# Optimization experiments

Measured on AMD Instinct MI355X. Metric: run time of the kernel, lower is better.

The kernel has to match this reference:

```python
import jax, jax.numpy as jnp
import numpy as np

HEADS = 8
AGENT = 49
POOL = 7   # sqrt(AGENT)
WIN = 32


def _adaptive_avg_pool(x, out):
    # x: (b, h, w, c) -> (b, out, out, c), replicating torch AdaptiveAvgPool2d bins
    h = x.shape[1]
    starts = [(i * h) // out for i in range(out)]
    ends = [-((-(i + 1) * h) // out) for i in range(out)]
    rows = jnp.stack([x[:, s:e].mean(axis=1) for s, e in zip(starts, ends)], axis=1)      # (b,out,w,c)
    return jnp.stack([rows[:, :, s:e].mean(axis=2) for s, e in zip(starts, ends)], axis=2)  # (b,out,out,c)


def setup_inputs() -> dict:
    key = jax.random.key(0)
    ks = jax.random.split(key, 13)
    b, n, c = 32, WIN * WIN, 256
    std = 0.02
    return {
        "x": jax.random.normal(ks[0], (b, n + 1, c), jnp.float32),
        "qkv_w": jax.random.normal(ks[1], (3 * c, c), jnp.float32) * std,
        "proj_w": jax.random.normal(ks[2], (c, c), jnp.float32) * std,
        "proj_b": jnp.zeros((c,), jnp.float32),
        "dwc_w": jax.random.normal(ks[3], (c, 1, 3, 3), jnp.float32) * std,  # torch (C_out, 1, kh, kw)
        "dwc_b": jnp.zeros((c,), jnp.float32),
        "an_bias": jax.random.normal(ks[4], (HEADS, AGENT, 7, 7), jnp.float32) * std,
        "ah_bias": jax.random.normal(ks[5], (1, HEADS, AGENT, WIN, 1), jnp.float32) * std,
        "aw_bias": jax.random.normal(ks[6], (1, HEADS, AGENT, 1, WIN), jnp.float32) * std,
        "na_bias": jax.random.normal(ks[7], (HEADS, AGENT, 7, 7), jnp.float32) * std,
        "ha_bias": jax.random.normal(ks[8], (1, HEADS, WIN, 1, AGENT), jnp.float32) * std,
        "wa_bias": jax.random.normal(ks[9], (1, HEADS, 1, WIN, AGENT), jnp.float32) * std,
    }


def reference(x, qkv_w, proj_w, proj_b, dwc_w, dwc_b,
              an_bias, ah_bias, aw_bias, na_bias, ha_bias, wa_bias):
    cls_tok, xs = x[:, :1], x[:, 1:]
    b, n, c = xs.shape
    h = w = WIN
    hd = c // HEADS
    scale = hd ** -0.5

    qkv = xs @ qkv_w.T                                   # (b, n, 3c)
    q, k, v = jnp.split(qkv, 3, axis=-1)                 # each (b, n, c)

    # agent tokens: adaptive avg pool of q over the spatial grid
    agents = _adaptive_avg_pool(q.reshape(b, h, w, c), POOL).reshape(b, AGENT, c)

    qh = q.reshape(b, n, HEADS, hd).transpose(0, 2, 1, 3)        # (b,H,n,d)
    kh = k.reshape(b, n, HEADS, hd).transpose(0, 2, 1, 3)
    vh = v.reshape(b, n, HEADS, hd).transpose(0, 2, 1, 3)
    ah = agents.reshape(b, AGENT, HEADS, hd).transpose(0, 2, 1, 3)  # (b,H,A,d)

    # stage 1: agent <-> k/v, bias interpolated 7x7 -> WINxWIN (half-pixel bilinear == torch align_corners=False)
    pb1 = jax.image.resize(an_bias, (HEADS, AGENT, WIN, WIN), method='bilinear').reshape(1, HEADS, AGENT, n)
    pb2 = (ah_bias + aw_bias).reshape(1, HEADS, AGENT, n)
    agent_attn = jax.nn.softmax((ah * scale) @ kh.transpose(0, 1, 3, 2) + pb1 + pb2, axis=-1)  # (b,H,A,n)
    agent_v = agent_attn @ vh                                    # (b,H,A,d)

    # stage 2: q <-> agents
    ab1 = jax.image.resize(na_bias, (HEADS, AGENT, WIN, WIN), method='bilinear').reshape(1, HEADS, AGENT, n).transpose(0, 1, 3, 2)
    ab2 = (ha_bias + wa_bias).reshape(1, HEADS, n, AGENT)
    q_attn = jax.nn.softmax((qh * scale) @ ah.transpose(0, 1, 3, 2) + ab1 + ab2, axis=-1)      # (b,H,n,A)
    out = (q_attn @ agent_v).transpose(0, 2, 1, 3).reshape(b, n, c)

    # depthwise conv residual on v (NHWC)
    v_img = vh.transpose(0, 2, 1, 3).reshape(b, h, w, c)
    kern = dwc_w.transpose(2, 3, 1, 0)                            # (3,3,1,c) HWIO
    dwc = jax.lax.conv_general_dilated(v_img, kern, (1, 1), 'SAME',
                                       feature_group_count=c,
                                       dimension_numbers=('NHWC', 'HWIO', 'NHWC')) + dwc_b
    out = out + dwc.reshape(b, n, c)

    out = jnp.concatenate([cls_tok, out], axis=1)
    return out @ proj_w.T + proj_b
```

## Files before the change

kernel.cpp:

```cpp
#include <hip/hip_runtime.h>
#include <hip/hip_bf16.h>

#define BATCH 32
#define NTOK 1024
#define CH 256
#define HEADS 8
#define HD 32
#define AGENTS 49
#define WIN 32
#define QKV_N 768
#define SCALE 0.17677669529663687f

typedef unsigned short u16;
typedef __attribute__((ext_vector_type(8))) unsigned short u16x8;
typedef __attribute__((ext_vector_type(8))) short short8;
typedef __attribute__((ext_vector_type(4))) float f32x4;

__device__ __forceinline__ void gload_lds16(const void* g, const void* l) {
    __builtin_amdgcn_global_load_lds(
        (const __attribute__((address_space(1))) unsigned int*)g,
        (__attribute__((address_space(3))) unsigned int*)l, 16, 0, 0);
}

__device__ __forceinline__ u16 f2bf1(float f) {
    unsigned u = __builtin_bit_cast(unsigned, f);
    u += 0x7fffu + ((u >> 16) & 1u);
    return (u16)(u >> 16);
}
__device__ __forceinline__ float bf2f(u16 v) {
    unsigned u = ((unsigned)v) << 16;
    return __builtin_bit_cast(float, u);
}

__global__ void f2bf_kernel(const float* __restrict__ in, u16* __restrict__ out, int n8) {
    int i = blockIdx.x * 256 + threadIdx.x;
    if (i >= n8) return;
    float4 v0 = ((const float4*)in)[i * 2];
    float4 v1 = ((const float4*)in)[i * 2 + 1];
    u16x8 o;
    o[0] = f2bf1(v0.x); o[1] = f2bf1(v0.y); o[2] = f2bf1(v0.z); o[3] = f2bf1(v0.w);
    o[4] = f2bf1(v1.x); o[5] = f2bf1(v1.y); o[6] = f2bf1(v1.z); o[7] = f2bf1(v1.w);
    ((u16x8*)out)[i] = o;
}

__global__ __launch_bounds__(256) void gemm_bf16(const u16* __restrict__ A,
                                                 const u16* __restrict__ B,
                                                 float* __restrict__ C,
                                                 u16* __restrict__ C16,
                                                 int M, int N, int K,
                                                 const float* __restrict__ bias,
                                                 int amode) {
    __shared__ u16 As[128 * 32];
    __shared__ u16 Bs[128 * 32];
    const int tid = threadIdx.x;
    const int lane = tid & 63;
    const int wid = tid >> 6;
    const int row0 = blockIdx.x * 128, col0 = blockIdx.y * 128;
    const int wr = wid >> 1, wc = wid & 1;
    const int fr = lane & 15, fq = lane >> 4;

    f32x4 acc[4][4];
#pragma unroll
    for (int m = 0; m < 4; ++m)
#pragma unroll
        for (int n = 0; n < 4; ++n) acc[m][n] = (f32x4)(0.f);

    for (int k0 = 0; k0 < K; k0 += 32) {
#pragma unroll
        for (int r = 0; r < 2; ++r) {
            int trow = (tid >> 2) + r * 64;
            int tcol = (tid & 3) * 8;
            size_t aoff;
            int grow = row0 + trow;
            if (amode == 1) {
                int bb = grow >> 10, nn = grow & 1023;
                aoff = ((size_t)(bb * 1025 + nn + 1)) * 256 + (size_t)(k0 + tcol);
            } else {
                if (grow >= M) grow = M - 1;
                aoff = (size_t)grow * K + (size_t)(k0 + tcol);
            }
            gload_lds16(A + aoff, (const char*)As + wid * 1024 + r * 4096);
            int brow = col0 + trow;
            gload_lds16(B + (size_t)brow * K + (size_t)(k0 + tcol),
                        (const char*)Bs + wid * 1024 + r * 4096);
        }
        __syncthreads();

        short8 af[4], bf[4];
#pragma unroll
        for (int m = 0; m < 4; ++m)
            af[m] = *(const short8*)&As[(wr * 64 + m * 16 + fr) * 32 + fq * 8];
#pragma unroll
        for (int n = 0; n < 4; ++n)
            bf[n] = *(const short8*)&Bs[(wc * 64 + n * 16 + fr) * 32 + fq * 8];
#pragma unroll
        for (int m = 0; m < 4; ++m)
#pragma unroll
            for (int n = 0; n < 4; ++n)
                acc[m][n] = __builtin_amdgcn_mfma_f32_16x16x32_bf16(af[m], bf[n], acc[m][n], 0, 0, 0);
        __syncthreads();
    }

#pragma unroll
    for (int m = 0; m < 4; ++m) {
#pragma unroll
        for (int j = 0; j < 4; ++j) {
            int row = row0 + wr * 64 + m * 16 + fq * 4 + j;
            if (row < M) {
#pragma unroll
                for (int n = 0; n < 4; ++n) {
                    int col = col0 + wc * 64 + n * 16 + fr;
                    float v = acc[m][n][j];
                    if (bias) v += bias[col];
                    if (C16) C16[(size_t)row * N + col] = f2bf1(v);
                    else     C[(size_t)row * N + col] = v;
                }
            }
        }
    }
}

__global__ __launch_bounds__(256) void pool_kernel(const u16* __restrict__ qkvb,
                                                   float* __restrict__ agents) {
    int b = blockIdx.x / 7, py = blockIdx.x % 7;
    int ch = threadIdx.x;
    int ys = py * 32 / 7, ye = ((py + 1) * 32 + 6) / 7;
    float acc[7];
#pragma unroll
    for (int i = 0; i < 7; ++i) acc[i] = 0.f;
    for (int y = ys; y < ye; ++y) {
        const u16* rowp = qkvb + ((size_t)(b * NTOK + y * 32)) * QKV_N + ch;
#pragma unroll
        for (int PX = 0; PX < 7; ++PX) {
            const int xs = PX * 32 / 7, xe = ((PX + 1) * 32 + 6) / 7;
            float s = 0.f;
            for (int x = xs; x < xe; ++x) s += bf2f(rowp[(size_t)x * QKV_N]);
            acc[PX] += s;
        }
    }
    int rcnt = ye - ys;
#pragma unroll
    for (int PX = 0; PX < 7; ++PX) {
        const int xs = PX * 32 / 7, xe = ((PX + 1) * 32 + 6) / 7;
        agents[((size_t)(b * AGENTS + py * 7 + PX)) * CH + ch] =
            acc[PX] / (float)(rcnt * (xe - xs));
    }
}

__device__ inline float bilin7(const float* __restrict__ m, float sy, float sx) {
    float fy0 = floorf(sy), fx0 = floorf(sx);
    int y0 = (int)fy0, x0 = (int)fx0;
    float fy = sy - fy0, fx = sx - fx0;
    int y0c = min(max(y0, 0), 6), y1c = min(max(y0 + 1, 0), 6);
    int x0c = min(max(x0, 0), 6), x1c = min(max(x0 + 1, 0), 6);
    float v00 = m[y0c * 7 + x0c], v01 = m[y0c * 7 + x1c];
    float v10 = m[y1c * 7 + x0c], v11 = m[y1c * 7 + x1c];
    return (1.f - fy) * ((1.f - fx) * v00 + fx * v01) + fy * ((1.f - fx) * v10 + fx * v11);
}

__global__ void pb_kernel(const float* __restrict__ an, const float* __restrict__ ahb,
                          const float* __restrict__ awb, float* __restrict__ pba) {
    int h = blockIdx.x / AGENTS, a = blockIdx.x % AGENTS;
    const float* m = an + (h * AGENTS + a) * 49;
    for (int n = threadIdx.x; n < NTOK; n += 256) {
        int y = n >> 5, x = n & 31;
        float v = bilin7(m, (y + 0.5f) * (7.f / 32.f) - 0.5f, (x + 0.5f) * (7.f / 32.f) - 0.5f);
        v += ahb[(h * AGENTS + a) * 32 + y] + awb[(h * AGENTS + a) * 32 + x];
        pba[((size_t)(h * AGENTS + a)) * NTOK + n] = v;
    }
}

__global__ void ab_kernel(const float* __restrict__ na, const float* __restrict__ hab,
                          const float* __restrict__ wab, float* __restrict__ ab) {
    int idx = blockIdx.x * 256 + threadIdx.x;
    if (idx >= HEADS * NTOK * AGENTS) return;
    int h = idx / (NTOK * AGENTS);
    int r = idx % (NTOK * AGENTS);
    int n = r / AGENTS, a = r % AGENTS;
    int y = n >> 5, x = n & 31;
    const float* m = na + (h * AGENTS + a) * 49;
    float v = bilin7(m, (y + 0.5f) * (7.f / 32.f) - 0.5f, (x + 0.5f) * (7.f / 32.f) - 0.5f);
    v += hab[(h * 32 + y) * AGENTS + a] + wab[(h * 32 + x) * AGENTS + a];
    ab[idx] = v;
}

__global__ __launch_bounds__(512) void agent_attn3(const u16* __restrict__ qkvb,
                                                   const float* __restrict__ agents,
                                                   const float* __restrict__ pba,
                                                   float* __restrict__ agent_v) {
    int b = blockIdx.x >> 3, h = blockIdx.x & 7;
    int tid = threadIdx.x, lane = tid & 63, w = tid >> 6;
    const int fr = lane & 15, fq = lane >> 4;

#define VTP 1038
    __shared__ u16 ah_lds[64 * 32];
    __shared__ u16 Vt[32 * VTP];
    __shared__ float PO[8][2304];
    __shared__ float lsum_lds[8][64];

    u16*   Pw = (u16*)&PO[w][0];
    float* Ow = &PO[w][0];

    for (int li = tid; li < 64 * 32; li += 512) {
        int a = li >> 5, d = li & 31;
        float v = (a < AGENTS) ? agents[((size_t)(b * AGENTS + a)) * CH + h * HD + d] * SCALE : 0.f;
        ah_lds[li] = f2bf1(v);
    }
    for (int li = tid; li < NTOK * 4; li += 512) {
        int tok = li >> 2, d8 = (li & 3) * 8;
        u16x8 v = *(const u16x8*)&qkvb[((size_t)(b * NTOK + tok)) * QKV_N + 2 * CH + h * HD + d8];
#pragma unroll
        for (int j = 0; j < 8; ++j) Vt[(d8 + j) * VTP + tok] = v[j];
    }
    __syncthreads();

    short8 ahf[4];
#pragma unroll
    for (int mt = 0; mt < 4; ++mt)
        ahf[mt] = *(const short8*)&ah_lds[(mt * 16 + fr) * 32 + fq * 8];

    float lsum[4][4];
#pragma unroll
    for (int mt = 0; mt < 4; ++mt)
#pragma unroll
        for (int j = 0; j < 4; ++j) lsum[mt][j] = 0.f;
    f32x4 accO[4][2];
#pragma unroll
    for (int mt = 0; mt < 4; ++mt)
#pragma unroll
        for (int ntd = 0; ntd < 2; ++ntd) accO[mt][ntd] = (f32x4)(0.f);

    const float* pbh = pba + (size_t)h * AGENTS * NTOK;

#pragma unroll
    for (int c2 = 0; c2 < 2; ++c2) {
        int tb = w * 128 + c2 * 64;
        short8 kf[4];
#pragma unroll
        for (int nt = 0; nt < 4; ++nt)
            kf[nt] = *(const short8*)&qkvb[((size_t)(b * NTOK + tb + nt * 16 + fr)) * QKV_N + CH + h * HD + fq * 8];

        f32x4 accS[4];
#pragma unroll
        for (int mt = 0; mt < 4; ++mt) {
#pragma unroll
            for (int nt = 0; nt < 4; ++nt)
                accS[nt] = __builtin_amdgcn_mfma_f32_16x16x32_bf16(ahf[mt], kf[nt], (f32x4)(0.f), 0, 0, 0);
#pragma unroll
            for (int j = 0; j < 4; ++j) {
                int a = mt * 16 + fq * 4 + j;
                const float* pbrow = pbh + (size_t)min(a, AGENTS - 1) * NTOK + tb;
#pragma unroll
                for (int nt = 0; nt < 4; ++nt) {
                    float e = __expf(accS[nt][j] + pbrow[nt * 16 + fr]);
                    lsum[mt][j] += e;
                    Pw[a * 72 + nt * 16 + fr] = f2bf1(e);
                }
            }
        }

        asm volatile("s_waitcnt lgkmcnt(0)" ::: "memory");
        __builtin_amdgcn_sched_barrier(0);

        short8 pf[4][2], vf[2][2];
#pragma unroll
        for (int mt = 0; mt < 4; ++mt)
#pragma unroll
            for (int kc = 0; kc < 2; ++kc)
                pf[mt][kc] = *(const short8*)&Pw[(mt * 16 + fr) * 72 + kc * 32 + fq * 8];
#pragma unroll
        for (int ntd = 0; ntd < 2; ++ntd)
#pragma unroll
            for (int kc = 0; kc < 2; ++kc)
                vf[ntd][kc] = *(const short8*)&Vt[(ntd * 16 + fr) * VTP + tb + kc * 32 + fq * 8];

        asm volatile("s_waitcnt lgkmcnt(0)" ::: "memory");
        __builtin_amdgcn_sched_barrier(0);

#pragma unroll
        for (int mt = 0; mt < 4; ++mt)
#pragma unroll
            for (int kc = 0; kc < 2; ++kc)
#pragma unroll
                for (int ntd = 0; ntd < 2; ++ntd)
                    accO[mt][ntd] = __builtin_amdgcn_mfma_f32_16x16x32_bf16(pf[mt][kc], vf[ntd][kc], accO[mt][ntd], 0, 0, 0);
    }

#pragma unroll
    for (int mt = 0; mt < 4; ++mt)
#pragma unroll
        for (int j = 0; j < 4; ++j) {
            float s = lsum[mt][j];
            s += __shfl_xor(s, 1);
            s += __shfl_xor(s, 2);
            s += __shfl_xor(s, 4);
            s += __shfl_xor(s, 8);
            lsum[mt][j] = s;
        }
    if (fr == 0) {
#pragma unroll
        for (int mt = 0; mt < 4; ++mt)
#pragma unroll
            for (int j = 0; j < 4; ++j)
                lsum_lds[w][mt * 16 + fq * 4 + j] = lsum[mt][j];
    }

#pragma unroll
    for (int mt = 0; mt < 4; ++mt)
#pragma unroll
        for (int ntd = 0; ntd < 2; ++ntd)
#pragma unroll
            for (int j = 0; j < 4; ++j)
                Ow[(mt * 16 + fq * 4 + j) * 32 + ntd * 16 + fr] = accO[mt][ntd][j];

    asm volatile("s_waitcnt lgkmcnt(0)" ::: "memory");
    __syncthreads();

    for (int li = tid; li < AGENTS * HD; li += 512) {
        int a = li >> 5, d = li & 31;
        float L = 0.f, o = 0.f;
#pragma unroll
        for (int ww = 0; ww < 8; ++ww) {
            o += PO[ww][a * 32 + d];
            L += lsum_lds[ww][a];
        }
        agent_v[(((size_t)(b * HEADS + h)) * AGENTS + a) * HD + d] = o / L;
    }
#undef VTP
}

__global__ __launch_bounds__(256) void q_attn_dwc(const u16* __restrict__ qkvb,
                                                  const float* __restrict__ agents,
                                                  const float* __restrict__ agent_v,
                                                  const float* __restrict__ ab,
                                                  const float* __restrict__ dwc_w,
                                                  const float* __restrict__ dwc_b,
                                                  u16* __restrict__ outbf) {
    int blk = blockIdx.x;
    int b = blk / 32, rem = blk % 32;
    int h = rem / 4, ck = rem % 4;
    int tid = threadIdx.x;
    int w = tid >> 6, lane = tid & 63;
    int fr = lane & 15, fq = lane >> 4;
    int tb = ck * 256 + w * 64;

    __shared__ u16 Vs[10][32][40];
    __shared__ u16 ah_lds[64][32];
    __shared__ u16 avT[32][72];
    __shared__ u16 Pall[4][32 * 68];
    __shared__ float w9[9][32];
    __shared__ float bia[32];

    u16* Pw = &Pall[w][0];

    for (int li = tid; li < 64 * 32; li += 256) {
        int a = li >> 5, d = li & 31;
        float v = (a < AGENTS) ? agents[((size_t)(b * AGENTS + a)) * CH + h * HD + d] * SCALE : 0.f;
        ah_lds[a][d] = f2bf1(v);
    }
    for (int li = tid; li < 32 * 64; li += 256) {
        int d = li >> 6, a = li & 63;
        float v = (a < AGENTS) ? agent_v[(((size_t)(b * HEADS + h)) * AGENTS + a) * HD + d] : 0.f;
        avT[d][a] = f2bf1(v);
    }
    for (int li = tid; li < 288; li += 256) {
        int t = li >> 5, d = li & 31;
        w9[t][d] = dwc_w[(h * HD + d) * 9 + t];
    }
    if (tid < 32) bia[tid] = dwc_b[h * HD + tid];
    {
        int y0 = ck * 8 - 1;
#pragma unroll
        for (int it = 0; it < 5; ++it) {
            int c = it * 256 + tid;
            int r = c >> 7;
            int w7 = c & 127;
            int xx = w7 >> 2;
            int d8 = (w7 & 3) * 8;
            int yy = y0 + r;
            u16x8 v = (u16x8)(0);
            if (yy >= 0 && yy < 32)
                v = *(const u16x8*)&qkvb[((size_t)(b * NTOK + yy * 32 + xx)) * QKV_N + 2 * CH + h * HD + d8];
            *(u16x8*)&Vs[r][xx][d8] = v;
        }
    }
    __syncthreads();

    short8 ahf[4];
#pragma unroll
    for (int nt = 0; nt < 4; ++nt)
        ahf[nt] = *(const short8*)&ah_lds[nt * 16 + fr][fq * 8];
    short8 avf[2][2];
#pragma unroll
    for (int ntd = 0; ntd < 2; ++ntd)
#pragma unroll
        for (int kc = 0; kc < 2; ++kc)
            avf[ntd][kc] = *(const short8*)&avT[ntd * 16 + fr][kc * 32 + fq * 8];

    const float* abh = ab + (size_t)h * NTOK * AGENTS;

#pragma unroll
    for (int half = 0; half < 2; ++half) {
        int hb = tb + half * 32;

#pragma unroll
        for (int mt2 = 0; mt2 < 2; ++mt2) {
            int tok = hb + mt2 * 16 + fr;
            short8 qf = *(const short8*)(qkvb + ((size_t)(b * NTOK + tok)) * QKV_N + h * HD + fq * 8);
            f32x4 accS[4];
#pragma unroll
            for (int nt = 0; nt < 4; ++nt)
                accS[nt] = __builtin_amdgcn_mfma_f32_16x16x32_bf16(qf, ahf[nt], (f32x4)(0.f), 0, 0, 0);

            float e[4][4];
            float ps[4];
#pragma unroll
            for (int j = 0; j < 4; ++j) ps[j] = 0.f;
#pragma unroll
            for (int j = 0; j < 4; ++j) {
                int tkj = hb + mt2 * 16 + fq * 4 + j;
                const float* abrow = abh + (size_t)tkj * AGENTS;
#pragma unroll
                for (int nt = 0; nt < 4; ++nt) {
                    int a = nt * 16 + fr;
                    float s = accS[nt][j] + abrow[min(a, AGENTS - 1)];
                    float ev = (a < AGENTS) ? __expf(s) : 0.f;
                    e[j][nt] = ev;
                    ps[j] += ev;
                }
            }
#pragma unroll
            for (int j = 0; j < 4; ++j) {
                ps[j] += __shfl_xor(ps[j], 1);
                ps[j] += __shfl_xor(ps[j], 2);
                ps[j] += __shfl_xor(ps[j], 4);
                ps[j] += __shfl_xor(ps[j], 8);
            }
#pragma unroll
            for (int j = 0; j < 4; ++j) {
                float inv = 1.f / ps[j];
                int tl = mt2 * 16 + fq * 4 + j;
#pragma unroll
                for (int nt = 0; nt < 4; ++nt)
                    Pw[tl * 68 + nt * 16 + fr] = f2bf1(e[j][nt] * inv);
            }
        }

        asm volatile("s_waitcnt lgkmcnt(0)" ::: "memory");
        __builtin_amdgcn_sched_barrier(0);

        short8 pf[2][2];
#pragma unroll
        for (int mt2 = 0; mt2 < 2; ++mt2)
#pragma unroll
            for (int kc = 0; kc < 2; ++kc)
                pf[mt2][kc] = *(const short8*)&Pw[(mt2 * 16 + fr) * 68 + kc * 32 + fq * 8];

        asm volatile("s_waitcnt lgkmcnt(0)" ::: "memory");
        __builtin_amdgcn_sched_barrier(0);

        f32x4 accO[2][2];
#pragma unroll
        for (int mt2 = 0; mt2 < 2; ++mt2)
#pragma unroll
            for (int ntd = 0; ntd < 2; ++ntd) accO[mt2][ntd] = (f32x4)(0.f);
#pragma unroll
        for (int mt2 = 0; mt2 < 2; ++mt2)
#pragma unroll
            for (int kc = 0; kc < 2; ++kc)
#pragma unroll
                for (int ntd = 0; ntd < 2; ++ntd)
                    accO[mt2][ntd] = __builtin_amdgcn_mfma_f32_16x16x32_bf16(pf[mt2][kc], avf[ntd][kc], accO[mt2][ntd], 0, 0, 0);

        int y = ck * 8 + w * 2 + half;
        int lr = w * 2 + half + 1;
#pragma unroll
        for (int ntd = 0; ntd < 2; ++ntd) {
            int d = ntd * 16 + fr;
            float wv[9];
#pragma unroll
            for (int t = 0; t < 9; ++t) wv[t] = w9[t][d];
            float bv = bia[d];
#pragma unroll
            for (int mt2 = 0; mt2 < 2; ++mt2) {
                int x0 = mt2 * 16 + fq * 4;
                float vv[3][6];
#pragma unroll
                for (int dy = 0; dy < 3; ++dy)
#pragma unroll
                    for (int k = 0; k < 6; ++k) {
                        int xx = x0 - 1 + k;
                        vv[dy][k] = (xx >= 0 && xx < 32) ? bf2f(Vs[lr - 1 + dy][xx][d]) : 0.f;
                    }
#pragma unroll
                for (int j = 0; j < 4; ++j) {
                    float o = accO[mt2][ntd][j] + bv;
#pragma unroll
                    for (int dy = 0; dy < 3; ++dy)
#pragma unroll
                        for (int dx = 0; dx < 3; ++dx)
                            o = fmaf(wv[dy * 3 + dx], vv[dy][j + dx], o);
                    int n = y * 32 + x0 + j;
                    outbf[((size_t)(b * 1025 + 1 + n)) * CH + h * HD + d] = f2bf1(o);
                }
            }
        }
    }
}

extern "C" void kernel_launch(void* const* d_in, const int* in_sizes, int n_in,
                              void* d_out, int out_size, void* d_ws, size_t ws_size,
                              hipStream_t stream) {
    const float* x      = (const float*)d_in[0];
    const float* qkv_w  = (const float*)d_in[1];
    const float* proj_w = (const float*)d_in[2];
    const float* proj_b = (const float*)d_in[3];
    const float* dwc_w  = (const float*)d_in[4];
    const float* dwc_b  = (const float*)d_in[5];
    const float* an_b   = (const float*)d_in[6];
    const float* ah_b   = (const float*)d_in[7];
    const float* aw_b   = (const float*)d_in[8];
    const float* na_b   = (const float*)d_in[9];
    const float* ha_b   = (const float*)d_in[10];
    const float* wa_b   = (const float*)d_in[11];
    float* out = (float*)d_out;

    float* ws      = (float*)d_ws;
    u16*   qkvb    = (u16*)ws;
    float* agents  = ws + 12582912;
    float* pba     = agents + 401408;
    float* ab      = pba + 401408;
    float* agent_v = ab + 401408;
    u16* xbf  = (u16*)(agent_v + 401408);
    u16* qwbf = xbf + 8396800;
    u16* pwbf = qwbf + 196608;

    f2bf_kernel<<<4100, 256, 0, stream>>>(x, xbf, 8396800 / 8);
    f2bf_kernel<<<96, 256, 0, stream>>>(qkv_w, qwbf, 196608 / 8);
    f2bf_kernel<<<32, 256, 0, stream>>>(proj_w, pwbf, 65536 / 8);
    gemm_bf16<<<dim3(256, 6), 256, 0, stream>>>(xbf, qwbf, nullptr, qkvb, 32768, 768, 256, nullptr, 1);
    pool_kernel<<<BATCH * 7, 256, 0, stream>>>(qkvb, agents);
    pb_kernel<<<HEADS * AGENTS, 256, 0, stream>>>(an_b, ah_b, aw_b, pba);
    ab_kernel<<<(HEADS * NTOK * AGENTS + 255) / 256, 256, 0, stream>>>(na_b, ha_b, wa_b, ab);
    agent_attn3<<<BATCH * HEADS, 512, 0, stream>>>(qkvb, agents, pba, agent_v);
    q_attn_dwc<<<BATCH * HEADS * 4, 256, 0, stream>>>(qkvb, agents, agent_v, ab, dwc_w, dwc_b, xbf);
    gemm_bf16<<<dim3(257, 2), 256, 0, stream>>>(xbf, pwbf, out, nullptr, 32800, 256, 256, proj_b, 0);
}
```

Before: 146.3 us.

## Fuse agent attention and query attention with depthwise conv into one kernel

After: 135.6 us. 7.3% less time.

```diff
diff --git a/kernel.cpp b/kernel.cpp
--- a/kernel.cpp
+++ b/kernel.cpp
@@ -171,32 +171,38 @@
 }
 
 __global__ void ab_kernel(const float* __restrict__ na, const float* __restrict__ hab,
-                          const float* __restrict__ wab, float* __restrict__ ab) {
+                          const float* __restrict__ wab, float* __restrict__ abT) {
     int idx = blockIdx.x * 256 + threadIdx.x;
-    if (idx >= HEADS * NTOK * AGENTS) return;
-    int h = idx / (NTOK * AGENTS);
-    int r = idx % (NTOK * AGENTS);
-    int n = r / AGENTS, a = r % AGENTS;
+    if (idx >= HEADS * AGENTS * NTOK) return;
+    int h = idx / (AGENTS * NTOK);
+    int r = idx % (AGENTS * NTOK);
+    int a = r / NTOK, n = r % NTOK;
     int y = n >> 5, x = n & 31;
     const float* m = na + (h * AGENTS + a) * 49;
     float v = bilin7(m, (y + 0.5f) * (7.f / 32.f) - 0.5f, (x + 0.5f) * (7.f / 32.f) - 0.5f);
     v += hab[(h * 32 + y) * AGENTS + a] + wab[(h * 32 + x) * AGENTS + a];
-    ab[idx] = v;
-}
-
-__global__ __launch_bounds__(512) void agent_attn3(const u16* __restrict__ qkvb,
-                                                   const float* __restrict__ agents,
-                                                   const float* __restrict__ pba,
-                                                   float* __restrict__ agent_v) {
+    abT[idx] = v;
+}
+
+#define VTP 1038
+__global__ __launch_bounds__(512) void fused_attn(const u16* __restrict__ qkvb,
+                                                  const float* __restrict__ agents,
+                                                  const float* __restrict__ pba,
+                                                  const float* __restrict__ abT,
+                                                  const float* __restrict__ dwc_w,
+                                                  const float* __restrict__ dwc_b,
+                                                  u16* __restrict__ outbf) {
     int b = blockIdx.x >> 3, h = blockIdx.x & 7;
     int tid = threadIdx.x, lane = tid & 63, w = tid >> 6;
     const int fr = lane & 15, fq = lane >> 4;
 
-#define VTP 1038
     __shared__ u16 ah_lds[64 * 32];
     __shared__ u16 Vt[32 * VTP];
     __shared__ float PO[8][2304];
     __shared__ float lsum_lds[8][64];
+    __shared__ u16 avT[32][72];
+    __shared__ float w9[9][32];
+    __shared__ float bia[32];
 
     u16*   Pw = (u16*)&PO[w][0];
     float* Ow = &PO[w][0];
@@ -212,6 +218,11 @@
 #pragma unroll
         for (int j = 0; j < 8; ++j) Vt[(d8 + j) * VTP + tok] = v[j];
     }
+    for (int li = tid; li < 288; li += 512) {
+        int t = li >> 5, d = li & 31;
+        w9[t][d] = dwc_w[(h * HD + d) * 9 + t];
+    }
+    if (tid < 32) bia[tid] = dwc_b[h * HD + tid];
     __syncthreads();
 
     short8 ahf[4];
@@ -224,11 +235,11 @@
     for (int mt = 0; mt < 4; ++mt)
 #pragma unroll
         for (int j = 0; j < 4; ++j) lsum[mt][j] = 0.f;
-    f32x4 accO[4][2];
+    f32x4 accA[4][2];
 #pragma unroll
     for (int mt = 0; mt < 4; ++mt)
 #pragma unroll
-        for (int ntd = 0; ntd < 2; ++ntd) accO[mt][ntd] = (f32x4)(0.f);
+        for (int ntd = 0; ntd < 2; ++ntd) accA[mt][ntd] = (f32x4)(0.f);
 
     const float* pbh = pba + (size_t)h * AGENTS * NTOK;
 
@@ -283,7 +294,7 @@
             for (int kc = 0; kc < 2; ++kc)
 #pragma unroll
                 for (int ntd = 0; ntd < 2; ++ntd)
-                    accO[mt][ntd] = __builtin_amdgcn_mfma_f32_16x16x32_bf16(pf[mt][kc], vf[ntd][kc], accO[mt][ntd], 0, 0, 0);
+                    accA[mt][ntd] = __builtin_amdgcn_mfma_f32_16x16x32_bf16(pf[mt][kc], vf[ntd][kc], accA[mt][ntd], 0, 0, 0);
     }
 
 #pragma unroll
@@ -311,85 +322,27 @@
         for (int ntd = 0; ntd < 2; ++ntd)
 #pragma unroll
             for (int j = 0; j < 4; ++j)
-                Ow[(mt * 16 + fq * 4 + j) * 32 + ntd * 16 + fr] = accO[mt][ntd][j];
+                Ow[(mt * 16 + fq * 4 + j) * 32 + ntd * 16 + fr] = accA[mt][ntd][j];
 
     asm volatile("s_waitcnt lgkmcnt(0)" ::: "memory");
     __syncthreads();
 
-    for (int li = tid; li < AGENTS * HD; li += 512) {
-        int a = li >> 5, d = li & 31;
-        float L = 0.f, o = 0.f;
-#pragma unroll
-        for (int ww = 0; ww < 8; ++ww) {
-            o += PO[ww][a * 32 + d];
-            L += lsum_lds[ww][a];
-        }
-        agent_v[(((size_t)(b * HEADS + h)) * AGENTS + a) * HD + d] = o / L;
-    }
-#undef VTP
-}
-
-__global__ __launch_bounds__(256) void q_attn_dwc(const u16* __restrict__ qkvb,
-                                                  const float* __restrict__ agents,
-                                                  const float* __restrict__ agent_v,
-                                                  const float* __restrict__ ab,
-                                                  const float* __restrict__ dwc_w,
-                                                  const float* __restrict__ dwc_b,
-                                                  u16* __restrict__ outbf) {
-    int blk = blockIdx.x;
-    int b = blk / 32, rem = blk % 32;
-    int h = rem / 4, ck = rem % 4;
-    int tid = threadIdx.x;
-    int w = tid >> 6, lane = tid & 63;
-    int fr = lane & 15, fq = lane >> 4;
-    int tb = ck * 256 + w * 64;
-
-    __shared__ u16 Vs[10][32][40];
-    __shared__ u16 ah_lds[64][32];
-    __shared__ u16 avT[32][72];
-    __shared__ u16 Pall[4][32 * 68];
-    __shared__ float w9[9][32];
-    __shared__ float bia[32];
-
-    u16* Pw = &Pall[w][0];
-
-    for (int li = tid; li < 64 * 32; li += 256) {
-        int a = li >> 5, d = li & 31;
-        float v = (a < AGENTS) ? agents[((size_t)(b * AGENTS + a)) * CH + h * HD + d] * SCALE : 0.f;
-        ah_lds[a][d] = f2bf1(v);
-    }
-    for (int li = tid; li < 32 * 64; li += 256) {
-        int d = li >> 6, a = li & 63;
-        float v = (a < AGENTS) ? agent_v[(((size_t)(b * HEADS + h)) * AGENTS + a) * HD + d] : 0.f;
-        avT[d][a] = f2bf1(v);
-    }
-    for (int li = tid; li < 288; li += 256) {
-        int t = li >> 5, d = li & 31;
-        w9[t][d] = dwc_w[(h * HD + d) * 9 + t];
-    }
-    if (tid < 32) bia[tid] = dwc_b[h * HD + tid];
-    {
-        int y0 = ck * 8 - 1;
-#pragma unroll
-        for (int it = 0; it < 5; ++it) {
-            int c = it * 256 + tid;
-            int r = c >> 7;
-            int w7 = c & 127;
-            int xx = w7 >> 2;
-            int d8 = (w7 & 3) * 8;
-            int yy = y0 + r;
-            u16x8 v = (u16x8)(0);
-            if (yy >= 0 && yy < 32)
-                v = *(const u16x8*)&qkvb[((size_t)(b * NTOK + yy * 32 + xx)) * QKV_N + 2 * CH + h * HD + d8];
-            *(u16x8*)&Vs[r][xx][d8] = v;
-        }
+    for (int li = tid; li < 64 * HD; li += 512) {
+        int a = li & 63, d = li >> 6;
+        float val = 0.f;
+        if (a < AGENTS) {
+            float L = 0.f, o = 0.f;
+#pragma unroll
+            for (int ww = 0; ww < 8; ++ww) {
+                o += PO[ww][a * 32 + d];
+                L += lsum_lds[ww][a];
+            }
+            val = o / L;
+        }
+        avT[d][a] = f2bf1(val);
     }
     __syncthreads();
 
-    short8 ahf[4];
-#pragma unroll
-    for (int nt = 0; nt < 4; ++nt)
-        ahf[nt] = *(const short8*)&ah_lds[nt * 16 + fr][fq * 8];
     short8 avf[2][2];
 #pragma unroll
     for (int ntd = 0; ntd < 2; ++ntd)
@@ -397,20 +350,23 @@
         for (int kc = 0; kc < 2; ++kc)
             avf[ntd][kc] = *(const short8*)&avT[ntd * 16 + fr][kc * 32 + fq * 8];
 
-    const float* abh = ab + (size_t)h * NTOK * AGENTS;
-
-#pragma unroll
-    for (int half = 0; half < 2; ++half) {
-        int hb = tb + half * 32;
+    const float* abTh = abT + (size_t)h * AGENTS * NTOK;
+
+#pragma unroll
+    for (int hh = 0; hh < 4; ++hh) {
+        int hb = w * 128 + hh * 32;
 
 #pragma unroll
         for (int mt2 = 0; mt2 < 2; ++mt2) {
             int tok = hb + mt2 * 16 + fr;
             short8 qf = *(const short8*)(qkvb + ((size_t)(b * NTOK + tok)) * QKV_N + h * HD + fq * 8);
             f32x4 accS[4];
-#pragma unroll
-            for (int nt = 0; nt < 4; ++nt)
+            f32x4 abv[4];
+#pragma unroll
+            for (int nt = 0; nt < 4; ++nt) {
                 accS[nt] = __builtin_amdgcn_mfma_f32_16x16x32_bf16(qf, ahf[nt], (f32x4)(0.f), 0, 0, 0);
+                abv[nt] = *(const f32x4*)&abTh[(size_t)min(nt * 16 + fr, AGENTS - 1) * NTOK + hb + mt2 * 16 + fq * 4];
+            }
 
             float e[4][4];
             float ps[4];
@@ -418,12 +374,10 @@
             for (int j = 0; j < 4; ++j) ps[j] = 0.f;
 #pragma unroll
             for (int j = 0; j < 4; ++j) {
-                int tkj = hb + mt2 * 16 + fq * 4 + j;
-                const float* abrow = abh + (size_t)tkj * AGENTS;
 #pragma unroll
                 for (int nt = 0; nt < 4; ++nt) {
                     int a = nt * 16 + fr;
-                    float s = accS[nt][j] + abrow[min(a, AGENTS - 1)];
+                    float s = accS[nt][j] + abv[nt][j];
                     float ev = (a < AGENTS) ? __expf(s) : 0.f;
                     e[j][nt] = ev;
                     ps[j] += ev;
@@ -449,12 +403,12 @@
         asm volatile("s_waitcnt lgkmcnt(0)" ::: "memory");
         __builtin_amdgcn_sched_barrier(0);
 
-        short8 pf[2][2];
+        short8 pf2[2][2];
 #pragma unroll
         for (int mt2 = 0; mt2 < 2; ++mt2)
 #pragma unroll
             for (int kc = 0; kc < 2; ++kc)
-                pf[mt2][kc] = *(const short8*)&Pw[(mt2 * 16 + fr) * 68 + kc * 32 + fq * 8];
+                pf2[mt2][kc] = *(const short8*)&Pw[(mt2 * 16 + fr) * 68 + kc * 32 + fq * 8];
 
         asm volatile("s_waitcnt lgkmcnt(0)" ::: "memory");
         __builtin_amdgcn_sched_barrier(0);
@@ -470,10 +424,9 @@
             for (int kc = 0; kc < 2; ++kc)
 #pragma unroll
                 for (int ntd = 0; ntd < 2; ++ntd)
-                    accO[mt2][ntd] = __builtin_amdgcn_mfma_f32_16x16x32_bf16(pf[mt2][kc], avf[ntd][kc], accO[mt2][ntd], 0, 0, 0);
-
-        int y = ck * 8 + w * 2 + half;
-        int lr = w * 2 + half + 1;
+                    accO[mt2][ntd] = __builtin_amdgcn_mfma_f32_16x16x32_bf16(pf2[mt2][kc], avf[ntd][kc], accO[mt2][ntd], 0, 0, 0);
+
+        int y = w * 4 + hh;
 #pragma unroll
         for (int ntd = 0; ntd < 2; ++ntd) {
             int d = ntd * 16 + fr;
@@ -481,17 +434,21 @@
 #pragma unroll
             for (int t = 0; t < 9; ++t) wv[t] = w9[t][d];
             float bv = bia[d];
+            const u16* Vd = &Vt[d * VTP];
 #pragma unroll
             for (int mt2 = 0; mt2 < 2; ++mt2) {
                 int x0 = mt2 * 16 + fq * 4;
                 float vv[3][6];
 #pragma unroll
-                for (int dy = 0; dy < 3; ++dy)
+                for (int dy = 0; dy < 3; ++dy) {
+                    int yy = y - 1 + dy;
 #pragma unroll
                     for (int k = 0; k < 6; ++k) {
                         int xx = x0 - 1 + k;
-                        vv[dy][k] = (xx >= 0 && xx < 32) ? bf2f(Vs[lr - 1 + dy][xx][d]) : 0.f;
+                        vv[dy][k] = (yy >= 0 && yy < 32 && xx >= 0 && xx < 32)
+                                  ? bf2f(Vd[yy * 32 + xx]) : 0.f;
                     }
+                }
 #pragma unroll
                 for (int j = 0; j < 4; ++j) {
                     float o = accO[mt2][ntd][j] + bv;
@@ -507,6 +464,7 @@
         }
     }
 }
+#undef VTP
 
 extern "C" void kernel_launch(void* const* d_in, const int* in_sizes, int n_in,
                               void* d_out, int out_size, void* d_ws, size_t ws_size,
@@ -529,9 +487,9 @@
     u16*   qkvb    = (u16*)ws;
     float* agents  = ws + 12582912;
     float* pba     = agents + 401408;
-    float* ab      = pba + 401408;
-    float* agent_v = ab + 401408;
-    u16* xbf  = (u16*)(agent_v + 401408);
+    float* abT     = pba + 401408;
+    float* unused  = abT + 401408;
+    u16* xbf  = (u16*)(unused + 401408);
     u16* qwbf = xbf + 8396800;
     u16* pwbf = qwbf + 196608;
 
@@ -541,8 +499,7 @@
     gemm_bf16<<<dim3(256, 6), 256, 0, stream>>>(xbf, qwbf, nullptr, qkvb, 32768, 768, 256, nullptr, 1);
     pool_kernel<<<BATCH * 7, 256, 0, stream>>>(qkvb, agents);
     pb_kernel<<<HEADS * AGENTS, 256, 0, stream>>>(an_b, ah_b, aw_b, pba);
-    ab_kernel<<<(HEADS * NTOK * AGENTS + 255) / 256, 256, 0, stream>>>(na_b, ha_b, wa_b, ab);
-    agent_attn3<<<BATCH * HEADS, 512, 0, stream>>>(qkvb, agents, pba, agent_v);
-    q_attn_dwc<<<BATCH * HEADS * 4, 256, 0, stream>>>(qkvb, agents, agent_v, ab, dwc_w, dwc_b, xbf);
+    ab_kernel<<<(HEADS * AGENTS * NTOK + 255) / 256, 256, 0, stream>>>(na_b, ha_b, wa_b, abT);
+    fused_attn<<<BATCH * HEADS, 512, 0, stream>>>(qkvb, agents, pba, abT, dwc_w, dwc_b, xbf);
     gemm_bf16<<<dim3(257, 2), 256, 0, stream>>>(xbf, pwbf, out, nullptr, 32800, 256, 256, proj_b, 0);
 }
```
